# Optimization experiments

Hardware: AMD Instinct MI355X
Metric: run time of the kernel (lower is better)

The kernel has to match this reference:

```python
import jax, jax.numpy as jnp
import numpy as np

V = 32000      # vocab_size
E = 256        # ModelConfig.n_embed
T_BLOCK = 2048 # ModelConfig.block_size
H = 4          # n_head (hardcoded in Bigram)
L = 3          # number of Blocks
HS = E // H    # head_size
EPS = 1e-5

def _ln(x, g, b):
    mu = jnp.mean(x, axis=-1, keepdims=True)
    var = jnp.var(x, axis=-1, keepdims=True)
    return (x - mu) * jax.lax.rsqrt(var + EPS) * g + b

def setup_inputs() -> dict:
    key = jax.random.key(0)
    ks = jax.random.split(key, 16)
    s = 0.02
    inp = {
        "idx": jax.random.randint(ks[0], (4, T_BLOCK), 0, V),
        "tok_emb": jax.random.normal(ks[1], (V, E), jnp.float32) * s,
        "pos_emb": jax.random.normal(ks[2], (T_BLOCK, E), jnp.float32) * s,
        # per-layer stacked params (heads concatenated -> full ExE projections)
        "Wq": jax.random.normal(ks[3], (L, E, E), jnp.float32) * s,
        "Wk": jax.random.normal(ks[4], (L, E, E), jnp.float32) * s,
        "Wv": jax.random.normal(ks[5], (L, E, E), jnp.float32) * s,
        "Wproj": jax.random.normal(ks[6], (L, E, E), jnp.float32) * s,
        "bproj": jnp.zeros((L, E), jnp.float32),
        "ln1_g": jnp.ones((L, E), jnp.float32),
        "ln1_b": jnp.zeros((L, E), jnp.float32),
        "W1": jax.random.normal(ks[7], (L, E, 4 * E), jnp.float32) * s,
        "b1": jnp.zeros((L, 4 * E), jnp.float32),
        "W2": jax.random.normal(ks[8], (L, 4 * E, E), jnp.float32) * s,
        "b2": jnp.zeros((L, E), jnp.float32),
        "ln2_g": jnp.ones((L, E), jnp.float32),
        "ln2_b": jnp.zeros((L, E), jnp.float32),
        "Wlm": jax.random.normal(ks[9], (E, V), jnp.float32) * s,
        "blm": jnp.zeros((V,), jnp.float32),
    }
    return inp

def reference(idx, tok_emb, pos_emb, Wq, Wk, Wv, Wproj, bproj, ln1_g, ln1_b,
              W1, b1, W2, b2, ln2_g, ln2_b, Wlm, blm):
    B, T = idx.shape
    x = tok_emb[idx] + pos_emb[:T]  # [B,T,E]
    causal = jnp.tril(jnp.ones((T, T), bool))
    # NOTE: source scales by C**0.5 with C = n_embed (not head_size)
    scale = 1.0 / jnp.sqrt(jnp.float32(E))
    for l in range(L):
        h = _ln(x, ln1_g[l], ln1_b[l])
        q = (h @ Wq[l]).reshape(B, T, H, HS).transpose(0, 2, 1, 3)
        k = (h @ Wk[l]).reshape(B, T, H, HS).transpose(0, 2, 1, 3)
        v = (h @ Wv[l]).reshape(B, T, H, HS).transpose(0, 2, 1, 3)
        wei = jnp.einsum('bhtd,bhsd->bhts', q, k) * scale
        wei = jnp.where(causal, wei, -jnp.inf)
        wei = jax.nn.softmax(wei, axis=-1)
        y = jnp.einsum('bhts,bhsd->bhtd', wei, v)
        y = y.transpose(0, 2, 1, 3).reshape(B, T, E)
        x = x + y @ Wproj[l] + bproj[l]
        h2 = _ln(x, ln2_g[l], ln2_b[l])
        x = x + jax.nn.relu(h2 @ W1[l] + b1[l]) @ W2[l] + b2[l]
    # ln_f exists in __init__ but is never applied in forward — skipped.
    logits = x @ Wlm + blm  # [B,T,V]
    return logits
```

## Files before the change

kernel.cpp:

```cpp
#include <hip/hip_runtime.h>
#include <hip/hip_bf16.h>

#define EMB 256
#define NHEAD 4
#define HSZ 64
#define NLAYER 3
#define TBLK 2048
#define VOCAB 32000
#define BATCH 4
#define LNEPS 1e-5f
#define BT (BATCH * TBLK)
#define QKVD (3 * EMB)

typedef __attribute__((ext_vector_type(8))) short bf16x8v;
typedef __attribute__((ext_vector_type(4))) float f32x4;
typedef unsigned short u16;
typedef unsigned int u32;

__device__ __forceinline__ u16 f2bf(float f) {
    union { float f; u32 u; } c; c.f = f;
    u32 r = c.u + 0x7fff + ((c.u >> 16) & 1);
    return (u16)(r >> 16);
}
__device__ __forceinline__ u32 pack2(float a, float b) {
    return (u32)f2bf(a) | ((u32)f2bf(b) << 16);
}

__device__ __forceinline__ void gload16(const u16* g, u16* l) {
    __builtin_amdgcn_global_load_lds(
        (__attribute__((address_space(1))) void*)g,
        (__attribute__((address_space(3))) void*)l, 16, 0, 0);
}

__global__ __launch_bounds__(256) void embed_ln_kernel(
    const int* __restrict__ idx, const float* __restrict__ tok,
    const float* __restrict__ pos, const float* __restrict__ g,
    const float* __restrict__ b, float* __restrict__ x, u16* __restrict__ hb)
{
    const int row = blockIdx.x * 4 + (threadIdx.x >> 6);
    const int t = row & (TBLK - 1);
    const int token = idx[row];
    const int e = (threadIdx.x & 63) * 4;
    const float4 tv = *(const float4*)&tok[(size_t)token * EMB + e];
    const float4 pv = *(const float4*)&pos[(size_t)t * EMB + e];
    float4 xv;
    xv.x = tv.x + pv.x; xv.y = tv.y + pv.y; xv.z = tv.z + pv.z; xv.w = tv.w + pv.w;
    *(float4*)&x[(size_t)row * EMB + e] = xv;

    float s1 = xv.x + xv.y + xv.z + xv.w;
    float s2 = xv.x * xv.x + xv.y * xv.y + xv.z * xv.z + xv.w * xv.w;
    #pragma unroll
    for (int off = 32; off >= 1; off >>= 1) {
        s1 += __shfl_xor(s1, off);
        s2 += __shfl_xor(s2, off);
    }
    const float mu  = s1 * (1.0f / EMB);
    const float var = s2 * (1.0f / EMB) - mu * mu;
    const float rs  = rsqrtf(var + LNEPS);
    const float4 gv = *(const float4*)&g[e];
    const float4 bv = *(const float4*)&b[e];
    ushort4 o;
    o.x = f2bf((xv.x - mu) * rs * gv.x + bv.x);
    o.y = f2bf((xv.y - mu) * rs * gv.y + bv.y);
    o.z = f2bf((xv.z - mu) * rs * gv.z + bv.z);
    o.w = f2bf((xv.w - mu) * rs * gv.w + bv.w);
    *(ushort4*)&hb[(size_t)row * EMB + e] = o;
}

__global__ __launch_bounds__(256) void ln_kernel(
    const float* __restrict__ x, const float* __restrict__ g,
    const float* __restrict__ b, u16* __restrict__ out)
{
    const int row = blockIdx.x * 4 + (threadIdx.x >> 6);
    const int e = (threadIdx.x & 63) * 4;
    const float4 xv = *(const float4*)&x[(size_t)row * EMB + e];
    float s1 = xv.x + xv.y + xv.z + xv.w;
    float s2 = xv.x * xv.x + xv.y * xv.y + xv.z * xv.z + xv.w * xv.w;
    #pragma unroll
    for (int off = 32; off >= 1; off >>= 1) {
        s1 += __shfl_xor(s1, off);
        s2 += __shfl_xor(s2, off);
    }
    const float mu  = s1 * (1.0f / EMB);
    const float var = s2 * (1.0f / EMB) - mu * mu;
    const float rs  = rsqrtf(var + LNEPS);
    const float4 gv = *(const float4*)&g[e];
    const float4 bv = *(const float4*)&b[e];
    ushort4 o;
    o.x = f2bf((xv.x - mu) * rs * gv.x + bv.x);
    o.y = f2bf((xv.y - mu) * rs * gv.y + bv.y);
    o.z = f2bf((xv.z - mu) * rs * gv.z + bv.z);
    o.w = f2bf((xv.w - mu) * rs * gv.w + bv.w);
    *(ushort4*)&out[(size_t)row * EMB + e] = o;
}

__global__ __launch_bounds__(256) void transpose_cast(
    const float* __restrict__ W, u16* __restrict__ Wt, int K, int N,
    size_t sW, size_t sWt)
{
    __shared__ float t[32][33];
    W  += (size_t)blockIdx.z * sW;
    Wt += (size_t)blockIdx.z * sWt;
    const int bx = blockIdx.x, by = blockIdx.y;
    const int tx = threadIdx.x, ty = threadIdx.y;
    #pragma unroll
    for (int i = 0; i < 32; i += 8)
        t[ty + i][tx] = W[(size_t)(by * 32 + ty + i) * N + bx * 32 + tx];
    __syncthreads();
    #pragma unroll
    for (int i = 0; i < 32; i += 8)
        Wt[(size_t)(bx * 32 + ty + i) * K + by * 32 + tx] = f2bf(t[tx][ty + i]);
}

__global__ __launch_bounds__(256) void transpose_qkvp(
    const float* __restrict__ Wq, const float* __restrict__ Wk,
    const float* __restrict__ Wv, const float* __restrict__ Wp,
    u16* __restrict__ Wqkvt, u16* __restrict__ Wprojt)
{
    __shared__ float t[32][33];
    const int which = blockIdx.z & 3, l = blockIdx.z >> 2;
    const float* W;
    u16* Wt;
    switch (which) {
        case 0: W = Wq + (size_t)l*EMB*EMB; Wt = Wqkvt + (size_t)l*QKVD*EMB;               break;
        case 1: W = Wk + (size_t)l*EMB*EMB; Wt = Wqkvt + (size_t)l*QKVD*EMB + EMB*EMB;     break;
        case 2: W = Wv + (size_t)l*EMB*EMB; Wt = Wqkvt + (size_t)l*QKVD*EMB + 2*EMB*EMB;   break;
        default:W = Wp + (size_t)l*EMB*EMB; Wt = Wprojt + (size_t)l*EMB*EMB;               break;
    }
    const int bx = blockIdx.x, by = blockIdx.y;
    const int tx = threadIdx.x, ty = threadIdx.y;
    #pragma unroll
    for (int i = 0; i < 32; i += 8)
        t[ty + i][tx] = W[(size_t)(by * 32 + ty + i) * EMB + bx * 32 + tx];
    __syncthreads();
    #pragma unroll
    for (int i = 0; i < 32; i += 8)
        Wt[(size_t)(bx * 32 + ty + i) * EMB + by * 32 + tx] = f2bf(t[tx][ty + i]);
}

template<int BNT, int BIAS, int RES, int RELU, int OUTBF>
__global__ __launch_bounds__(256) void mgemm(
    const u16* __restrict__ A, const u16* __restrict__ Bt,
    const float* __restrict__ bias, const float* __restrict__ res,
    void* __restrict__ Cv, int M, int N, int K)
{
    constexpr int MI = (BNT == 128) ? 4 : 2;
    __shared__ u16 Al[2][128 * 32];
    __shared__ u16 Bl[2][BNT * 32];
    const int tid = threadIdx.x;
    const int bm = blockIdx.x, bn = blockIdx.y;
    const int wid = tid >> 6, lane = tid & 63;
    const int wr = (BNT == 128) ? (wid >> 1) * 64 : wid * 32;
    const int wc = (BNT == 128) ? (wid & 1) * 64 : 0;
    const int fr = lane & 15, fq = lane >> 4;

    const int l4 = lane >> 2;
    const int lc_src = ((lane & 3) ^ ((l4 >> 1) & 3)) * 8;
    const u16* Aga = A  + (size_t)(bm * 128 + wid * 16 + l4) * K + lc_src;
    const u16* Bga = Bt + (size_t)(bn * BNT + wid * 16 + l4) * K + lc_src;
    const int lin = (wid * 16 + l4) * 32 + (lane & 3) * 8;

    const int rsw = (fq ^ ((fr >> 1) & 3)) * 8;

    f32x4 acc[MI][4];
    #pragma unroll
    for (int i = 0; i < MI; ++i)
        #pragma unroll
        for (int j = 0; j < 4; ++j)
            acc[i][j] = f32x4{0.f, 0.f, 0.f, 0.f};

    gload16(Aga,                  &Al[0][lin]);
    gload16(Aga + (size_t)64 * K, &Al[0][lin + 64 * 32]);
    gload16(Bga,                  &Bl[0][lin]);
    if (BNT == 128) gload16(Bga + (size_t)64 * K, &Bl[0][lin + 64 * 32]);

    int buf = 0;
    for (int k0 = 0; k0 < K; k0 += 32, buf ^= 1) {
        __syncthreads();
        if (k0 + 32 < K) {
            gload16(Aga + k0 + 32,                  &Al[buf ^ 1][lin]);
            gload16(Aga + (size_t)64 * K + k0 + 32, &Al[buf ^ 1][lin + 64 * 32]);
            gload16(Bga + k0 + 32,                  &Bl[buf ^ 1][lin]);
            if (BNT == 128)
                gload16(Bga + (size_t)64 * K + k0 + 32, &Bl[buf ^ 1][lin + 64 * 32]);
        }
        bf16x8v af[MI], bfr[4];
        #pragma unroll
        for (int mi = 0; mi < MI; ++mi)
            af[mi] = *(const bf16x8v*)&Al[buf][(wr + mi * 16 + fr) * 32 + rsw];
        #pragma unroll
        for (int ni = 0; ni < 4; ++ni)
            bfr[ni] = *(const bf16x8v*)&Bl[buf][(wc + ni * 16 + fr) * 32 + rsw];
        #pragma unroll
        for (int mi = 0; mi < MI; ++mi)
            #pragma unroll
            for (int ni = 0; ni < 4; ++ni)
                acc[mi][ni] = __builtin_amdgcn_mfma_f32_16x16x32_bf16(
                    af[mi], bfr[ni], acc[mi][ni], 0, 0, 0);
    }

    float* Cf = (float*)Cv;
    u16*   Cb = (u16*)Cv;
    #pragma unroll
    for (int mi = 0; mi < MI; ++mi) {
        #pragma unroll
        for (int j = 0; j < 4; ++j) {
            const int r = bm * 128 + wr + mi * 16 + fq * 4 + j;
            #pragma unroll
            for (int ni = 0; ni < 4; ++ni) {
                const int c = bn * BNT + wc + ni * 16 + fr;
                float v = acc[mi][ni][j];
                if (BIAS) v += bias[c];
                if (RELU) v = fmaxf(v, 0.f);
                if (RES)  v += res[(size_t)r * N + c];
                if (OUTBF) Cb[(size_t)r * N + c] = f2bf(v);
                else       Cf[(size_t)r * N + c] = v;
            }
        }
    }
}

template<int BIAS, int OUTBF>
__global__ __launch_bounds__(512) void mgemm_m256(
    const u16* __restrict__ A, const u16* __restrict__ Bt,
    const float* __restrict__ bias, void* __restrict__ Cv, int N, int K)
{
    __shared__ u16 Al[2][256 * 32];
    __shared__ u16 Bl[2][128 * 32];
    const int tid = threadIdx.x;
    const int bm = blockIdx.x, bn = blockIdx.y;
    const int wid = tid >> 6, lane = tid & 63;
    const int wr = (wid >> 1) * 64;
    const int wc = (wid & 1) * 64;
    const int fr = lane & 15, fq = lane >> 4;

    const int l4 = tid >> 2;
    const int ch = tid & 3;
    const int lc_src = (ch ^ ((l4 >> 1) & 3)) * 8;
    const u16* Aga = A  + (size_t)(bm * 256 + l4) * K + lc_src;
    const u16* Bga = Bt + (size_t)(bn * 128 + l4) * K + lc_src;
    const int lin = l4 * 32 + ch * 8;

    const int rsw = (fq ^ ((fr >> 1) & 3)) * 8;

    f32x4 acc[4][4];
    #pragma unroll
    for (int i = 0; i < 4; ++i)
        #pragma unroll
        for (int j = 0; j < 4; ++j)
            acc[i][j] = f32x4{0.f, 0.f, 0.f, 0.f};

    gload16(Aga,                   &Al[0][lin]);
    gload16(Aga + (size_t)128 * K, &Al[0][lin + 128 * 32]);
    gload16(Bga,                   &Bl[0][lin]);

    int buf = 0;
    for (int k0 = 0; k0 < K; k0 += 32, buf ^= 1) {
        __syncthreads();
        if (k0 + 32 < K) {
            gload16(Aga + k0 + 32,                   &Al[buf ^ 1][lin]);
            gload16(Aga + (size_t)128 * K + k0 + 32, &Al[buf ^ 1][lin + 128 * 32]);
            gload16(Bga + k0 + 32,                   &Bl[buf ^ 1][lin]);
        }
        bf16x8v af[4], bfr[4];
        #pragma unroll
        for (int mi = 0; mi < 4; ++mi)
            af[mi] = *(const bf16x8v*)&Al[buf][(wr + mi * 16 + fr) * 32 + rsw];
        #pragma unroll
        for (int ni = 0; ni < 4; ++ni)
            bfr[ni] = *(const bf16x8v*)&Bl[buf][(wc + ni * 16 + fr) * 32 + rsw];
        #pragma unroll
        for (int mi = 0; mi < 4; ++mi)
            #pragma unroll
            for (int ni = 0; ni < 4; ++ni)
                acc[mi][ni] = __builtin_amdgcn_mfma_f32_16x16x32_bf16(
                    af[mi], bfr[ni], acc[mi][ni], 0, 0, 0);
    }

    float* Cf = (float*)Cv;
    u16*   Cb = (u16*)Cv;
    #pragma unroll
    for (int mi = 0; mi < 4; ++mi) {
        #pragma unroll
        for (int j = 0; j < 4; ++j) {
            const int r = bm * 256 + wr + mi * 16 + fq * 4 + j;
            #pragma unroll
            for (int ni = 0; ni < 4; ++ni) {
                const int c = bn * 128 + wc + ni * 16 + fr;
                float v = acc[mi][ni][j];
                if (BIAS) v += bias[c];
                if (OUTBF) Cb[(size_t)r * N + c] = f2bf(v);
                else       Cf[(size_t)r * N + c] = v;
            }
        }
    }
}

__global__ __launch_bounds__(256) void attn_kernel(
    const u16* __restrict__ qkv, u16* __restrict__ y)
{
    constexpr int LDK = 72;
    __shared__ u16 Kl[2][64 * LDK];
    __shared__ u16 Vt[2][64 * LDK];

    const int tid = threadIdx.x;
    const int qt = (int)gridDim.x - 1 - (int)blockIdx.x;
    const int bh = blockIdx.y;
    const int b = bh >> 2, h = bh & 3;
    const int w = tid >> 6, lane = tid & 63;
    const int fr = lane & 15, fq = lane >> 4;
    const size_t rowbase = (size_t)b * TBLK;
    const int qoff = h * HSZ, koff = EMB + h * HSZ, voff = 2 * EMB + h * HSZ;
    const int qg = qt * 64 + w * 16 + fr;

    bf16x8v qf[2];
    #pragma unroll
    for (int ks = 0; ks < 2; ++ks)
        qf[ks] = *(const bf16x8v*)&qkv[(rowbase + qg) * QKVD + qoff + ks * 32 + fq * 8];

    f32x4 yac[4];
    #pragma unroll
    for (int mi = 0; mi < 4; ++mi) yac[mi] = f32x4{0.f, 0.f, 0.f, 0.f};
    float m = -1e30f, l = 0.f;

    const int skv = tid >> 2, sc = (tid & 3) * 16;
    const u16* kbase = &qkv[(rowbase + skv) * QKVD + koff + sc];
    const u16* vbase = &qkv[(rowbase + skv) * QKVD + voff + sc];

    bf16x8v kr0 = *(const bf16x8v*)kbase;
    bf16x8v kr1 = *(const bf16x8v*)(kbase + 8);
    bf16x8v vr0 = *(const bf16x8v*)vbase;
    bf16x8v vr1 = *(const bf16x8v*)(vbase + 8);

    int buf = 0;
    for (int kv0 = 0; kv0 <= qt * 64; kv0 += 64, buf ^= 1) {
        {
            u16* Kw = &Kl[buf][skv * LDK + sc];
            *(bf16x8v*)Kw = kr0; *(bf16x8v*)(Kw + 8) = kr1;
            #pragma unroll
            for (int i = 0; i < 8; ++i) Vt[buf][(sc + i) * LDK + skv] = (u16)vr0[i];
            #pragma unroll
            for (int i = 0; i < 8; ++i) Vt[buf][(sc + 8 + i) * LDK + skv] = (u16)vr1[i];
        }
        __syncthreads();
        if (kv0 + 64 <= qt * 64) {
            const size_t off = (size_t)(kv0 + 64) * QKVD;
            kr0 = *(const bf16x8v*)(kbase + off);
            kr1 = *(const bf16x8v*)(kbase + off + 8);
            vr0 = *(const bf16x8v*)(vbase + off);
            vr1 = *(const bf16x8v*)(vbase + off + 8);
        }

        f32x4 st[4];
        __builtin_amdgcn_s_setprio(1);
        #pragma unroll
        for (int mb = 0; mb < 4; ++mb) {
            st[mb] = f32x4{0.f, 0.f, 0.f, 0.f};
            #pragma unroll
            for (int ks = 0; ks < 2; ++ks) {
                const bf16x8v kf = *(const bf16x8v*)
                    &Kl[buf][(mb * 16 + fr) * LDK + ks * 32 + fq * 8];
                st[mb] = __builtin_amdgcn_mfma_f32_16x16x32_bf16(
                    kf, qf[ks], st[mb], 0, 0, 0);
            }
        }
        __builtin_amdgcn_s_setprio(0);
        float p[4][4];
        float mloc = -1e30f;
        #pragma unroll
        for (int mb = 0; mb < 4; ++mb)
            #pragma unroll
            for (int j = 0; j < 4; ++j) {
                const int kvg = kv0 + mb * 16 + fq * 4 + j;
                const float s = (kvg <= qg) ? st[mb][j] * 0.0625f : -1e30f;
                p[mb][j] = s;
                mloc = fmaxf(mloc, s);
            }
        mloc = fmaxf(mloc, __shfl_xor(mloc, 16));
        mloc = fmaxf(mloc, __shfl_xor(mloc, 32));
        const float mnew = fmaxf(m, mloc);
        const float alpha = __expf(m - mnew);
        float rsum = 0.f;
        #pragma unroll
        for (int mb = 0; mb < 4; ++mb)
            #pragma unroll
            for (int j = 0; j < 4; ++j) {
                p[mb][j] = __expf(p[mb][j] - mnew);
                rsum += p[mb][j];
            }
        rsum += __shfl_xor(rsum, 16);
        rsum += __shfl_xor(rsum, 32);
        l = l * alpha + rsum;
        m = mnew;
        #pragma unroll
        for (int mi = 0; mi < 4; ++mi) yac[mi] *= alpha;

        u32 pk[4][2];
        #pragma unroll
        for (int mb = 0; mb < 4; ++mb) {
            pk[mb][0] = pack2(p[mb][0], p[mb][1]);
            pk[mb][1] = pack2(p[mb][2], p[mb][3]);
        }
        #pragma unroll
        for (int ksv = 0; ksv < 2; ++ksv) {
            union { u32 u[4]; bf16x8v v; } pf;
            #pragma unroll
            for (int t = 0; t < 4; ++t) {
                const int srcl = ((fq & 1) * 2 + (t >> 1)) * 16 + fr;
                const u32 lo = __shfl(pk[ksv * 2 + 0][t & 1], srcl);
                const u32 hi = __shfl(pk[ksv * 2 + 1][t & 1], srcl);
                pf.u[t] = (fq >> 1) ? hi : lo;
            }
            __builtin_amdgcn_s_setprio(1);
            #pragma unroll
            for (int mi = 0; mi < 4; ++mi) {
                const bf16x8v vf = *(const bf16x8v*)
                    &Vt[buf][(mi * 16 + fr) * LDK + ksv * 32 + fq * 8];
                yac[mi] = __builtin_amdgcn_mfma_f32_16x16x32_bf16(
                    vf, pf.v, yac[mi], 0, 0, 0);
            }
            __builtin_amdgcn_s_setprio(0);
        }
    }

    const float inv = 1.f / l;
    #pragma unroll
    for (int mi = 0; mi < 4; ++mi) {
        ushort4 o;
        o.x = f2bf(yac[mi][0] * inv);
        o.y = f2bf(yac[mi][1] * inv);
        o.z = f2bf(yac[mi][2] * inv);
        o.w = f2bf(yac[mi][3] * inv);
        *(ushort4*)&y[(rowbase + qg) * EMB + h * HSZ + mi * 16 + fq * 4] = o;
    }
}

extern "C" void kernel_launch(void* const* d_in, const int* in_sizes, int n_in,
                              void* d_out, int out_size, void* d_ws, size_t ws_size,
                              hipStream_t stream) {
    const int*   idx   = (const int*)  d_in[0];
    const float* tok   = (const float*)d_in[1];
    const float* pos   = (const float*)d_in[2];
    const float* Wq    = (const float*)d_in[3];
    const float* Wk    = (const float*)d_in[4];
    const float* Wv    = (const float*)d_in[5];
    const float* Wproj = (const float*)d_in[6];
    const float* bproj = (const float*)d_in[7];
    const float* ln1g  = (const float*)d_in[8];
    const float* ln1b  = (const float*)d_in[9];
    const float* W1    = (const float*)d_in[10];
    const float* b1    = (const float*)d_in[11];
    const float* W2    = (const float*)d_in[12];
    const float* b2    = (const float*)d_in[13];
    const float* ln2g  = (const float*)d_in[14];
    const float* ln2b  = (const float*)d_in[15];
    const float* Wlm   = (const float*)d_in[16];
    const float* blm   = (const float*)d_in[17];
    float* out = (float*)d_out;

    float* x    = (float*)d_ws;
    u16*   hb   = (u16*)(x + (size_t)BT * EMB);
    u16*   qkvb = hb + (size_t)BT * EMB;
    u16*   yb   = qkvb + (size_t)BT * QKVD;
    u16*   hid  = qkvb;
    u16*   Wqkvt  = yb + (size_t)BT * EMB;
    u16*   Wprojt = Wqkvt  + (size_t)NLAYER * QKVD * EMB;
    u16*   W1t    = Wprojt + (size_t)NLAYER * EMB * EMB;
    u16*   W2t    = W1t    + (size_t)NLAYER * EMB * 4 * EMB;
    u16*   Wlmt   = W2t    + (size_t)NLAYER * 4 * EMB * EMB;

    const dim3 tb(32, 8);
    transpose_qkvp<<<dim3(8, 8, NLAYER * 4), tb, 0, stream>>>(
        Wq, Wk, Wv, Wproj, Wqkvt, Wprojt);
    transpose_cast<<<dim3(32, 8, NLAYER), tb, 0, stream>>>(
        W1, W1t, EMB, 4*EMB, (size_t)EMB*4*EMB, (size_t)EMB*4*EMB);
    transpose_cast<<<dim3(8, 32, NLAYER), tb, 0, stream>>>(
        W2, W2t, 4*EMB, EMB, (size_t)4*EMB*EMB, (size_t)4*EMB*EMB);
    transpose_cast<<<dim3(VOCAB/32, 8, 1), tb, 0, stream>>>(
        Wlm, Wlmt, EMB, VOCAB, 0, 0);

    embed_ln_kernel<<<BT/4, 256, 0, stream>>>(idx, tok, pos, ln1g, ln1b, x, hb);

    for (int l = 0; l < NLAYER; ++l) {
        mgemm<128,0,0,0,1><<<dim3(BT/128, QKVD/128), 256, 0, stream>>>(
            hb, Wqkvt + (size_t)l*QKVD*EMB, nullptr, nullptr, qkvb, BT, QKVD, EMB);
        attn_kernel<<<dim3(TBLK/64, BATCH*NHEAD), 256, 0, stream>>>(qkvb, yb);
        mgemm<64,1,1,0,0><<<dim3(BT/128, EMB/64), 256, 0, stream>>>(
            yb, Wprojt + (size_t)l*EMB*EMB, bproj + l*EMB, x, x, BT, EMB, EMB);
        ln_kernel<<<BT/4, 256, 0, stream>>>(x, ln2g + l*EMB, ln2b + l*EMB, hb);
        mgemm<128,1,0,1,1><<<dim3(BT/128, 4*EMB/128), 256, 0, stream>>>(
            hb, W1t + (size_t)l*EMB*4*EMB, b1 + l*4*EMB, nullptr, hid, BT, 4*EMB, EMB);
        if (l < NLAYER - 1) {
            mgemm<64,1,1,0,0><<<dim3(BT/128, EMB/64), 256, 0, stream>>>(
                hid, W2t + (size_t)l*4*EMB*EMB, b2 + l*EMB, x, x, BT, EMB, 4*EMB);
            ln_kernel<<<BT/4, 256, 0, stream>>>(
                x, ln1g + (l+1)*EMB, ln1b + (l+1)*EMB, hb);
        } else {
            mgemm<64,1,1,0,1><<<dim3(BT/128, EMB/64), 256, 0, stream>>>(
                hid, W2t + (size_t)l*4*EMB*EMB, b2 + l*EMB, x, hb, BT, EMB, 4*EMB);
        }
    }

    mgemm_m256<1,0><<<dim3(BT/256, VOCAB/128), 512, 0, stream>>>(
        hb, Wlmt, blm, out, VOCAB, EMB);
}
```

Before: 682.1 us.

## Merge weight transposes into one launch, shrink GEMM tiles, use nontemporal logit stores

Combines the four weight transpose/cast launches into a single kernel that decodes which matrix each block handles from a flat block index, removing three kernel launches. Switches the QKV and FFN-up GEMMs from 128-wide to 64-wide N tiles, which doubles the number of workgroups so the CUs are better filled, at the cost of less reuse per tile. The LM-head GEMM now writes its fp32 logits with nontemporal stores so the large output stream pollutes the cache less.

```diff
diff --git a/kernel.cpp b/kernel.cpp
--- a/kernel.cpp
+++ b/kernel.cpp
@@ -94,14 +94,42 @@
     *(ushort4*)&out[(size_t)row * EMB + e] = o;
 }
 
-__global__ __launch_bounds__(256) void transpose_cast(
-    const float* __restrict__ W, u16* __restrict__ Wt, int K, int N,
-    size_t sW, size_t sWt)
+__global__ __launch_bounds__(256) void transpose_all(
+    const float* __restrict__ Wq, const float* __restrict__ Wk,
+    const float* __restrict__ Wv, const float* __restrict__ Wp,
+    const float* __restrict__ W1, const float* __restrict__ W2,
+    const float* __restrict__ Wlm,
+    u16* __restrict__ Wqkvt, u16* __restrict__ Wprojt, u16* __restrict__ W1t,
+    u16* __restrict__ W2t, u16* __restrict__ Wlmt)
 {
     __shared__ float t[32][33];
-    W  += (size_t)blockIdx.z * sW;
-    Wt += (size_t)blockIdx.z * sWt;
-    const int bx = blockIdx.x, by = blockIdx.y;
+    const int tb = blockIdx.x;
+    const float* W;
+    u16* Wt;
+    int K, N, bx, by;
+    if (tb < 768) {
+        const int z = tb >> 6, r = tb & 63;
+        const int which = z & 3, l = z >> 2;
+        switch (which) {
+            case 0: W = Wq + (size_t)l*EMB*EMB; Wt = Wqkvt + (size_t)l*QKVD*EMB;             break;
+            case 1: W = Wk + (size_t)l*EMB*EMB; Wt = Wqkvt + (size_t)l*QKVD*EMB + EMB*EMB;   break;
+            case 2: W = Wv + (size_t)l*EMB*EMB; Wt = Wqkvt + (size_t)l*QKVD*EMB + 2*EMB*EMB; break;
+            default:W = Wp + (size_t)l*EMB*EMB; Wt = Wprojt + (size_t)l*EMB*EMB;             break;
+        }
+        K = EMB; N = EMB; bx = r & 7; by = r >> 3;
+    } else if (tb < 1536) {
+        const int t2 = tb - 768, l = t2 >> 8, r = t2 & 255;
+        W = W1 + (size_t)l*EMB*4*EMB; Wt = W1t + (size_t)l*EMB*4*EMB;
+        K = EMB; N = 4*EMB; bx = r & 31; by = r >> 5;
+    } else if (tb < 2304) {
+        const int t2 = tb - 1536, l = t2 >> 8, r = t2 & 255;
+        W = W2 + (size_t)l*4*EMB*EMB; Wt = W2t + (size_t)l*4*EMB*EMB;
+        K = 4*EMB; N = EMB; bx = r & 7; by = r >> 3;
+    } else {
+        const int r = tb - 2304;
+        W = Wlm; Wt = Wlmt;
+        K = EMB; N = VOCAB; bx = r % 1000; by = r / 1000;
+    }
     const int tx = threadIdx.x, ty = threadIdx.y;
     #pragma unroll
     for (int i = 0; i < 32; i += 8)
@@ -110,32 +138,6 @@
     #pragma unroll
     for (int i = 0; i < 32; i += 8)
         Wt[(size_t)(bx * 32 + ty + i) * K + by * 32 + tx] = f2bf(t[tx][ty + i]);
-}
-
-__global__ __launch_bounds__(256) void transpose_qkvp(
-    const float* __restrict__ Wq, const float* __restrict__ Wk,
-    const float* __restrict__ Wv, const float* __restrict__ Wp,
-    u16* __restrict__ Wqkvt, u16* __restrict__ Wprojt)
-{
-    __shared__ float t[32][33];
-    const int which = blockIdx.z & 3, l = blockIdx.z >> 2;
-    const float* W;
-    u16* Wt;
-    switch (which) {
-        case 0: W = Wq + (size_t)l*EMB*EMB; Wt = Wqkvt + (size_t)l*QKVD*EMB;               break;
-        case 1: W = Wk + (size_t)l*EMB*EMB; Wt = Wqkvt + (size_t)l*QKVD*EMB + EMB*EMB;     break;
-        case 2: W = Wv + (size_t)l*EMB*EMB; Wt = Wqkvt + (size_t)l*QKVD*EMB + 2*EMB*EMB;   break;
-        default:W = Wp + (size_t)l*EMB*EMB; Wt = Wprojt + (size_t)l*EMB*EMB;               break;
-    }
-    const int bx = blockIdx.x, by = blockIdx.y;
-    const int tx = threadIdx.x, ty = threadIdx.y;
-    #pragma unroll
-    for (int i = 0; i < 32; i += 8)
-        t[ty + i][tx] = W[(size_t)(by * 32 + ty + i) * EMB + bx * 32 + tx];
-    __syncthreads();
-    #pragma unroll
-    for (int i = 0; i < 32; i += 8)
-        Wt[(size_t)(bx * 32 + ty + i) * EMB + by * 32 + tx] = f2bf(t[tx][ty + i]);
 }
 
 template<int BNT, int BIAS, int RES, int RELU, int OUTBF>
@@ -220,10 +222,10 @@
     }
 }
 
-template<int BIAS, int OUTBF>
+template<int BIAS>
 __global__ __launch_bounds__(512) void mgemm_m256(
     const u16* __restrict__ A, const u16* __restrict__ Bt,
-    const float* __restrict__ bias, void* __restrict__ Cv, int N, int K)
+    const float* __restrict__ bias, float* __restrict__ Cf, int N, int K)
 {
     __shared__ u16 Al[2][256 * 32];
     __shared__ u16 Bl[2][128 * 32];
@@ -277,8 +279,6 @@
                     af[mi], bfr[ni], acc[mi][ni], 0, 0, 0);
     }
 
-    float* Cf = (float*)Cv;
-    u16*   Cb = (u16*)Cv;
     #pragma unroll
     for (int mi = 0; mi < 4; ++mi) {
         #pragma unroll
@@ -289,8 +289,7 @@
                 const int c = bn * 128 + wc + ni * 16 + fr;
                 float v = acc[mi][ni][j];
                 if (BIAS) v += bias[c];
-                if (OUTBF) Cb[(size_t)r * N + c] = f2bf(v);
-                else       Cf[(size_t)r * N + c] = v;
+                __builtin_nontemporal_store(v, &Cf[(size_t)r * N + c]);
             }
         }
     }
@@ -469,26 +468,19 @@
     u16*   W2t    = W1t    + (size_t)NLAYER * EMB * 4 * EMB;
     u16*   Wlmt   = W2t    + (size_t)NLAYER * 4 * EMB * EMB;
 
-    const dim3 tb(32, 8);
-    transpose_qkvp<<<dim3(8, 8, NLAYER * 4), tb, 0, stream>>>(
-        Wq, Wk, Wv, Wproj, Wqkvt, Wprojt);
-    transpose_cast<<<dim3(32, 8, NLAYER), tb, 0, stream>>>(
-        W1, W1t, EMB, 4*EMB, (size_t)EMB*4*EMB, (size_t)EMB*4*EMB);
-    transpose_cast<<<dim3(8, 32, NLAYER), tb, 0, stream>>>(
-        W2, W2t, 4*EMB, EMB, (size_t)4*EMB*EMB, (size_t)4*EMB*EMB);
-    transpose_cast<<<dim3(VOCAB/32, 8, 1), tb, 0, stream>>>(
-        Wlm, Wlmt, EMB, VOCAB, 0, 0);
+    transpose_all<<<2304 + (VOCAB/32)*8, dim3(32, 8), 0, stream>>>(
+        Wq, Wk, Wv, Wproj, W1, W2, Wlm, Wqkvt, Wprojt, W1t, W2t, Wlmt);
 
     embed_ln_kernel<<<BT/4, 256, 0, stream>>>(idx, tok, pos, ln1g, ln1b, x, hb);
 
     for (int l = 0; l < NLAYER; ++l) {
-        mgemm<128,0,0,0,1><<<dim3(BT/128, QKVD/128), 256, 0, stream>>>(
+        mgemm<64,0,0,0,1><<<dim3(BT/128, QKVD/64), 256, 0, stream>>>(
             hb, Wqkvt + (size_t)l*QKVD*EMB, nullptr, nullptr, qkvb, BT, QKVD, EMB);
         attn_kernel<<<dim3(TBLK/64, BATCH*NHEAD), 256, 0, stream>>>(qkvb, yb);
         mgemm<64,1,1,0,0><<<dim3(BT/128, EMB/64), 256, 0, stream>>>(
             yb, Wprojt + (size_t)l*EMB*EMB, bproj + l*EMB, x, x, BT, EMB, EMB);
         ln_kernel<<<BT/4, 256, 0, stream>>>(x, ln2g + l*EMB, ln2b + l*EMB, hb);
-        mgemm<128,1,0,1,1><<<dim3(BT/128, 4*EMB/128), 256, 0, stream>>>(
+        mgemm<64,1,0,1,1><<<dim3(BT/128, 4*EMB/64), 256, 0, stream>>>(
             hb, W1t + (size_t)l*EMB*4*EMB, b1 + l*4*EMB, nullptr, hid, BT, 4*EMB, EMB);
         if (l < NLAYER - 1) {
             mgemm<64,1,1,0,0><<<dim3(BT/128, EMB/64), 256, 0, stream>>>(
@@ -501,6 +493,6 @@
         }
     }
 
-    mgemm_m256<1,0><<<dim3(BT/256, VOCAB/128), 512, 0, stream>>>(
+    mgemm_m256<1><<<dim3(BT/256, VOCAB/128), 512, 0, stream>>>(
         hb, Wlmt, blm, out, VOCAB, EMB);
 }
```

After: 635.2 us. -6.9%, faster.
